# Optimization experiments

Measured on AMD Instinct MI355X. Metric: run time of the kernel, lower is better.

Reference implementation:

```python
import jax, jax.numpy as jnp
import numpy as np

N, L, H, HEADS = 2, 2048, 1024, 16
HD = H // HEADS


def setup_inputs() -> dict:
    key = jax.random.key(0)
    ks = jax.random.split(key, 11)
    s = 1.0 / np.sqrt(H)  # torch Linear-ish init scale
    inp = {
        "H_q": jax.random.normal(ks[0], (N, L, H), jnp.float32),
        "H_k": jax.random.normal(ks[1], (N, L, H), jnp.float32),
        "H_v": jax.random.normal(ks[2], (N, L, H), jnp.float32),
        "W_q": jax.random.normal(ks[3], (H, H), jnp.float32) * s,
        "b_q": jax.random.normal(ks[4], (H,), jnp.float32) * s,
        "W_k": jax.random.normal(ks[5], (H, H), jnp.float32) * s,
        "b_k": jax.random.normal(ks[6], (H,), jnp.float32) * s,
        "W_v": jax.random.normal(ks[7], (H, H), jnp.float32) * s,
        "b_v": jax.random.normal(ks[8], (H,), jnp.float32) * s,
        "W_o": jax.random.normal(ks[9], (H, H), jnp.float32) * s,
        "b_o": jax.random.normal(ks[10], (H,), jnp.float32) * s,
        # causal lookahead mask (L, L): 1 where attending is allowed
        "mask": jnp.tril(jnp.ones((L, L), jnp.int32)),
    }
    return inp


def reference(H_q, H_k, H_v, W_q, b_q, W_k, b_k, W_v, b_v, W_o, b_o, mask):
    n = H_q.shape[0]
    scale = 1.0 / jnp.sqrt(jnp.asarray(H, H_q.dtype))
    # NOTE: faithful to original — raw reshape head split (no transpose),
    # and BOTH Q and K scaled by 1/sqrt(hidden_size).
    Q = ((H_q @ W_q + b_q) * scale).reshape(n, HEADS, L, HD)
    K = ((H_k @ W_k + b_k) * scale).reshape(n, HEADS, L, HD)
    V = (H_v @ W_v + b_v).reshape(n, HEADS, L, HD)
    sims = jnp.einsum("abic,abjc->abij", Q, K)  # (N, heads, L, L)
    neg_inf = jnp.asarray(-jnp.inf, sims.dtype)
    sims = jnp.where(mask[None, None, :, :] == 0, neg_inf, sims)
    # NOTE: softmax over axis=2 (the query axis i), as in the original.
    attn = jax.nn.softmax(sims, axis=2)
    contexts = jnp.einsum("abij,abjc->abic", attn, V)  # (N, heads, L, HD)
    concats = contexts.reshape(n, L, H)
    return concats @ W_o + b_o
```

## Files before the change

### kernel.cpp

```cpp
#include <hip/hip_runtime.h>

#define L 2048
#define HSZ 1024
#define HDIM 64

typedef float f32x4 __attribute__((ext_vector_type(4)));
typedef short short8v __attribute__((ext_vector_type(8)));

static __device__ __forceinline__ unsigned short f2bf(float f) {
    unsigned int u = __builtin_bit_cast(unsigned int, f);
    u += 0x7FFFu + ((u >> 16) & 1u);
    return (unsigned short)(u >> 16);
}
static __device__ __forceinline__ float bf2f(unsigned short u) {
    return __builtin_bit_cast(float, (unsigned int)u << 16);
}
static __device__ __forceinline__ unsigned int cvt_pk_bf16(float lo, float hi) {
    unsigned int r;
    asm("v_cvt_pk_bf16_f32 %0, %1, %2" : "=v"(r) : "v"(lo), "v"(hi));
    return r;
}
static __device__ __forceinline__ void gload_lds16(const void* g, void* l) {
    __builtin_amdgcn_global_load_lds(
        (const __attribute__((address_space(1))) unsigned int*)g,
        (__attribute__((address_space(3))) unsigned int*)l, 16, 0, 0);
}

__global__ __launch_bounds__(256) void wtrans_kernel(
    const float* __restrict__ W0, const float* __restrict__ W1,
    const float* __restrict__ W2, const float* __restrict__ W3,
    unsigned short* __restrict__ Wt4)
{
    const float* W;
    int z = blockIdx.z;
    if (z == 0) W = W0; else if (z == 1) W = W1; else if (z == 2) W = W2; else W = W3;
    unsigned short* T = Wt4 + (size_t)z * HSZ * HSZ;

    __shared__ __align__(16) unsigned short tl[64][72];
    int t = threadIdx.x;
    int k0 = blockIdx.y * 64, n0 = blockIdx.x * 64;

    int kl = t >> 2, nc = (t & 3) * 16;
    const float* src = W + (size_t)(k0 + kl) * HSZ + n0 + nc;
#pragma unroll
    for (int q = 0; q < 4; q++) {
        float4 v = ((const float4*)src)[q];
        tl[kl][nc + q * 4 + 0] = f2bf(v.x);
        tl[kl][nc + q * 4 + 1] = f2bf(v.y);
        tl[kl][nc + q * 4 + 2] = f2bf(v.z);
        tl[kl][nc + q * 4 + 3] = f2bf(v.w);
    }
    __syncthreads();
    int nl = t >> 2, kc = (t & 3) * 16;
    unsigned short tmp[16];
#pragma unroll
    for (int e = 0; e < 16; e++) tmp[e] = tl[kc + e][nl];
    unsigned short* dst = T + (size_t)(n0 + nl) * HSZ + k0 + kc;
    ((uint4*)dst)[0] = *(uint4*)&tmp[0];
    ((uint4*)dst)[1] = *(uint4*)&tmp[8];
}

__global__ __launch_bounds__(256) void hconv_kernel(
    const float* __restrict__ H0, const float* __restrict__ H1,
    const float* __restrict__ H2, unsigned short* __restrict__ Hbf)
{
    int z = blockIdx.y;
    const float* S = (z == 0) ? H0 : (z == 1) ? H1 : H2;
    size_t base = ((size_t)blockIdx.x * 256 + threadIdx.x) * 8;
    unsigned short* D = Hbf + (size_t)z * (4096 * 1024) + base;
    float4 a = *(const float4*)(S + base);
    float4 b = *(const float4*)(S + base + 4);
    unsigned short o[8] = {f2bf(a.x), f2bf(a.y), f2bf(a.z), f2bf(a.w),
                           f2bf(b.x), f2bf(b.y), f2bf(b.z), f2bf(b.w)};
    *(uint4*)D = *(const uint4*)o;
}

__global__ __launch_bounds__(256) void gemm_glds_kernel(
    const unsigned short* __restrict__ A, const unsigned short* __restrict__ B,
    const float* __restrict__ bias0, const float* __restrict__ bias1,
    const float* __restrict__ bias2, float scale01, float scale2,
    unsigned short* __restrict__ outbase)
{
    __shared__ __align__(16) unsigned short As[2][4096];
    __shared__ __align__(16) unsigned short Bs[2][4096];

    int raw = blockIdx.x;
    int xcd = raw & 7, idx = raw >> 3;
    int mb = (xcd * 4 + (idx & 3)) * 128;
    int col = idx >> 2;
    int proj = col >> 3;
    int nb = (col & 7) * 128;

    int t = threadIdx.x;
    int lane = t & 63, w = t >> 6;
    int lr = lane & 15, lg = lane >> 4;
    int wm = (w >> 1) * 64, wn = (w & 1) * 64;

    const unsigned short* Ap = A + (size_t)proj * (4096 * 1024);
    const unsigned short* Bp = B + (size_t)proj * (1024 * 1024);
    const float* bias = (proj == 0) ? bias0 : (proj == 1) ? bias1 : bias2;
    float scale = (proj < 2) ? scale01 : scale2;

    int c0 = w * 64 + lane;
    int r0 = c0 >> 2, e0 = (c0 & 3) * 8;
    int r1 = r0 + 64;
    const unsigned short* gA0 = Ap + (size_t)(mb + r0) * HSZ + e0;
    const unsigned short* gA1 = Ap + (size_t)(mb + r1) * HSZ + e0;
    const unsigned short* gB0 = Bp + (size_t)(nb + r0) * HSZ + e0;
    const unsigned short* gB1 = Bp + (size_t)(nb + r1) * HSZ + e0;

    f32x4 acc[4][4] = {};

    auto stage = [&](int buf, int kt) {
        gload_lds16(gA0 + kt, &As[buf][w * 512]);
        gload_lds16(gA1 + kt, &As[buf][2048 + w * 512]);
        gload_lds16(gB0 + kt, &Bs[buf][w * 512]);
        gload_lds16(gB1 + kt, &Bs[buf][2048 + w * 512]);
    };

    stage(0, 0);
    __syncthreads();

    int buf = 0;
    for (int kt = 0; kt < HSZ; kt += 32) {
        if (kt + 32 < HSZ) stage(buf ^ 1, kt + 32);

        short8v af[4], bfv[4];
#pragma unroll
        for (int s = 0; s < 4; s++) {
            af[s]  = *(const short8v*)&As[buf][(wm + s * 16 + lr) * 32 + lg * 8];
            bfv[s] = *(const short8v*)&Bs[buf][(wn + s * 16 + lr) * 32 + lg * 8];
        }
#pragma unroll
        for (int i = 0; i < 4; i++)
#pragma unroll
            for (int j = 0; j < 4; j++)
                acc[i][j] = __builtin_amdgcn_mfma_f32_16x16x32_bf16(af[i], bfv[j], acc[i][j], 0, 0, 0);
        __syncthreads();
        buf ^= 1;
    }

#pragma unroll
    for (int j = 0; j < 4; j++) {
        int colo = nb + wn + j * 16 + lr;
        float bv = bias[colo];
#pragma unroll
        for (int i = 0; i < 4; i++) {
            int row0 = mb + wm + i * 16 + lg * 4;
#pragma unroll
            for (int rg = 0; rg < 4; rg++) {
                float v = (acc[i][j][rg] + bv) * scale;
                outbase[(size_t)proj * (4096 * 1024) + (size_t)(row0 + rg) * HSZ + colo] = f2bf(v);
            }
        }
    }
}

__global__ __launch_bounds__(256) void gemm_o64_kernel(
    const unsigned short* __restrict__ A, const unsigned short* __restrict__ B,
    const float* __restrict__ bias, float* __restrict__ out)
{
    __shared__ __align__(16) unsigned short As[2][2048];
    __shared__ __align__(16) unsigned short Bs[2][4096];

    int raw = blockIdx.x;
    int xcd = raw & 7, idx = raw >> 3;
    int mb = (xcd * 8 + (idx & 7)) * 64;
    int nb = (idx >> 3) * 128;

    int t = threadIdx.x;
    int lane = t & 63, w = t >> 6;
    int lr = lane & 15, lg = lane >> 4;
    int wm = (w >> 1) * 32, wn = (w & 1) * 64;

    int c0 = w * 64 + lane;
    int r0 = c0 >> 2, e0 = (c0 & 3) * 8;
    const unsigned short* gA0 = A + (size_t)(mb + r0) * HSZ + e0;
    const unsigned short* gB0 = B + (size_t)(nb + r0) * HSZ + e0;
    const unsigned short* gB1 = B + (size_t)(nb + r0 + 64) * HSZ + e0;

    f32x4 acc[2][4] = {};

    auto stage = [&](int buf, int kt) {
        gload_lds16(gA0 + kt, &As[buf][w * 512]);
        gload_lds16(gB0 + kt, &Bs[buf][w * 512]);
        gload_lds16(gB1 + kt, &Bs[buf][2048 + w * 512]);
    };

    stage(0, 0);
    __syncthreads();

    int buf = 0;
    for (int kt = 0; kt < HSZ; kt += 32) {
        if (kt + 32 < HSZ) stage(buf ^ 1, kt + 32);

        short8v af[2], bfv[4];
#pragma unroll
        for (int s = 0; s < 2; s++)
            af[s]  = *(const short8v*)&As[buf][(wm + s * 16 + lr) * 32 + lg * 8];
#pragma unroll
        for (int s = 0; s < 4; s++)
            bfv[s] = *(const short8v*)&Bs[buf][(wn + s * 16 + lr) * 32 + lg * 8];
#pragma unroll
        for (int i = 0; i < 2; i++)
#pragma unroll
            for (int j = 0; j < 4; j++)
                acc[i][j] = __builtin_amdgcn_mfma_f32_16x16x32_bf16(af[i], bfv[j], acc[i][j], 0, 0, 0);
        __syncthreads();
        buf ^= 1;
    }

#pragma unroll
    for (int j = 0; j < 4; j++) {
        int colo = nb + wn + j * 16 + lr;
        float bv = bias[colo];
#pragma unroll
        for (int i = 0; i < 2; i++) {
            int row0 = mb + wm + i * 16 + lg * 4;
#pragma unroll
            for (int rg = 0; rg < 4; rg++)
                out[(size_t)(row0 + rg) * HSZ + colo] = acc[i][j][rg] + bv;
        }
    }
}

template<bool ABF16, bool OUTBF16>
__global__ __launch_bounds__(256) void gemm_bt_kernel(
    const void* __restrict__ Aptr, const unsigned short* __restrict__ Bt,
    const float* __restrict__ bias, float scale, void* __restrict__ outp)
{
    __shared__ __align__(16) unsigned short As[128][40];
    __shared__ __align__(16) unsigned short Bs[128][40];

    int t = threadIdx.x;
    int lane = t & 63, w = t >> 6;
    int lr = lane & 15, lg = lane >> 4;
    int mb = blockIdx.y * 128, nb = blockIdx.x * 128;
    int wm = (w >> 1) * 64, wn = (w & 1) * 64;
    int r = t >> 1, cc = (t & 1) * 16;

    f32x4 acc[4][4] = {};

    for (int kt = 0; kt < HSZ; kt += 32) {
        if (ABF16) {
            const unsigned short* A = (const unsigned short*)Aptr + (size_t)(mb + r) * HSZ + kt + cc;
            *(uint4*)&As[r][cc]     = ((const uint4*)A)[0];
            *(uint4*)&As[r][cc + 8] = ((const uint4*)A)[1];
        } else {
            const float* A = (const float*)Aptr + (size_t)(mb + r) * HSZ + kt + cc;
            unsigned short tmp[16];
#pragma unroll
            for (int q = 0; q < 4; q++) {
                float4 v = ((const float4*)A)[q];
                tmp[q * 4 + 0] = f2bf(v.x); tmp[q * 4 + 1] = f2bf(v.y);
                tmp[q * 4 + 2] = f2bf(v.z); tmp[q * 4 + 3] = f2bf(v.w);
            }
            *(uint4*)&As[r][cc]     = *(uint4*)&tmp[0];
            *(uint4*)&As[r][cc + 8] = *(uint4*)&tmp[8];
        }
        {
            const unsigned short* B = Bt + (size_t)(nb + r) * HSZ + kt + cc;
            *(uint4*)&Bs[r][cc]     = ((const uint4*)B)[0];
            *(uint4*)&Bs[r][cc + 8] = ((const uint4*)B)[1];
        }
        __syncthreads();

        short8v af[4], bf[4];
#pragma unroll
        for (int s = 0; s < 4; s++) af[s] = *(const short8v*)&As[wm + s * 16 + lr][8 * lg];
#pragma unroll
        for (int s = 0; s < 4; s++) bf[s] = *(const short8v*)&Bs[wn + s * 16 + lr][8 * lg];
#pragma unroll
        for (int i = 0; i < 4; i++)
#pragma unroll
            for (int j = 0; j < 4; j++)
                acc[i][j] = __builtin_amdgcn_mfma_f32_16x16x32_bf16(af[i], bf[j], acc[i][j], 0, 0, 0);
        __syncthreads();
    }

#pragma unroll
    for (int j = 0; j < 4; j++) {
        int col = nb + wn + j * 16 + lr;
        float bv = bias[col];
#pragma unroll
        for (int i = 0; i < 4; i++) {
            int row0 = mb + wm + i * 16 + lg * 4;
#pragma unroll
            for (int rg = 0; rg < 4; rg++) {
                float v = (acc[i][j][rg] + bv) * scale;
                if (OUTBF16)
                    ((unsigned short*)outp)[(size_t)(row0 + rg) * HSZ + col] = f2bf(v);
                else
                    ((float*)outp)[(size_t)(row0 + rg) * HSZ + col] = v;
            }
        }
    }
}

__global__ __launch_bounds__(256) void colsum_kernel(
    const unsigned short* __restrict__ Qb, const unsigned short* __restrict__ Kb,
    float* __restrict__ rcpC)
{
    int raw = blockIdx.x;
    int xcd = raw & 7, idx = raw >> 3;
    int head = xcd * 4 + (idx >> 5);
    int jbi = idx & 31;
    if ((idx >> 5) & 1) jbi = 31 - jbi;
    int jb = jbi * 64;
    const unsigned short* Qh = Qb + (size_t)head * L * HDIM;
    const unsigned short* Kh = Kb + (size_t)head * L * HDIM;
    int t = threadIdx.x, lane = t & 63, w = t >> 6;
    int lr = lane & 15, lg = lane >> 4;

    short8v af[4][2];
#pragma unroll
    for (int sj = 0; sj < 4; sj++)
#pragma unroll
        for (int kk = 0; kk < 2; kk++)
            af[sj][kk] = *(const short8v*)&Kh[(size_t)(jb + sj * 16 + lr) * HDIM + kk * 32 + 8 * lg];

    float accs[4][4] = {};

    int it0 = jb + w * 16;
    short8v bc0 = *(const short8v*)&Qh[(size_t)(it0 + lr) * HDIM + 8 * lg];
    short8v bc1 = *(const short8v*)&Qh[(size_t)(it0 + lr) * HDIM + 32 + 8 * lg];

    for (int it = it0; it < L; it += 64) {
        int itn = (it + 64 < L) ? it + 64 : it;
        short8v bn0 = *(const short8v*)&Qh[(size_t)(itn + lr) * HDIM + 8 * lg];
        short8v bn1 = *(const short8v*)&Qh[(size_t)(itn + lr) * HDIM + 32 + 8 * lg];
        if (it == it0) {
            int i = it + lr;
#pragma unroll
            for (int sj = 0; sj < 4; sj++) {
                f32x4 d = {0.0f, 0.0f, 0.0f, 0.0f};
                d = __builtin_amdgcn_mfma_f32_16x16x32_bf16(af[sj][0], bc0, d, 0, 0, 0);
                d = __builtin_amdgcn_mfma_f32_16x16x32_bf16(af[sj][1], bc1, d, 0, 0, 0);
#pragma unroll
                for (int rg = 0; rg < 4; rg++) {
                    int j = jb + sj * 16 + lg * 4 + rg;
                    if (i >= j) accs[sj][rg] += __expf(d[rg]);
                }
            }
        } else {
#pragma unroll
            for (int sj = 0; sj < 4; sj++) {
                f32x4 d = {0.0f, 0.0f, 0.0f, 0.0f};
                d = __builtin_amdgcn_mfma_f32_16x16x32_bf16(af[sj][0], bc0, d, 0, 0, 0);
                d = __builtin_amdgcn_mfma_f32_16x16x32_bf16(af[sj][1], bc1, d, 0, 0, 0);
#pragma unroll
                for (int rg = 0; rg < 4; rg++)
                    accs[sj][rg] += __expf(d[rg]);
            }
        }
        bc0 = bn0; bc1 = bn1;
    }

    __shared__ float part[4][64];
#pragma unroll
    for (int sj = 0; sj < 4; sj++)
#pragma unroll
        for (int rg = 0; rg < 4; rg++) {
            float v = accs[sj][rg];
            v += __shfl_xor(v, 1); v += __shfl_xor(v, 2);
            v += __shfl_xor(v, 4); v += __shfl_xor(v, 8);
            if (lr == 0) part[w][sj * 16 + lg * 4 + rg] = v;
        }
    __syncthreads();
    if (t < 64) {
        float s = part[0][t] + part[1][t] + part[2][t] + part[3][t];
        rcpC[(size_t)head * L + jb + t] = 1.0f / s;
    }
}

__global__ __launch_bounds__(256) void vtrans_kernel(
    const unsigned short* __restrict__ Vb, const float* __restrict__ rcpC,
    unsigned short* __restrict__ Vt)
{
    int p = blockIdx.y;
    int j0 = blockIdx.x * 64;
    const unsigned short* Vp = Vb + (size_t)p * L * HDIM;
    unsigned short* Tp = Vt + (size_t)p * HDIM * L;
    __shared__ __align__(16) unsigned short tl[64][72];
    int t = threadIdx.x;
    int jl = t >> 2, c0 = (t & 3) * 16;
    float rcv = rcpC[(size_t)p * L + j0 + jl];
    const unsigned short* src = Vp + (size_t)(j0 + jl) * HDIM + c0;
    unsigned short raw[16];
    *(uint4*)&raw[0] = ((const uint4*)src)[0];
    *(uint4*)&raw[8] = ((const uint4*)src)[1];
#pragma unroll
    for (int e = 0; e < 16; e++) tl[jl][c0 + e] = f2bf(bf2f(raw[e]) * rcv);
    __syncthreads();
    int cl = t >> 2, jc = (t & 3) * 16;
    unsigned short tmp[16];
#pragma unroll
    for (int e = 0; e < 16; e++) tmp[e] = tl[jc + e][cl];
    unsigned short* dst = Tp + (size_t)cl * L + j0 + jc;
    ((uint4*)dst)[0] = *(uint4*)&tmp[0];
    ((uint4*)dst)[1] = *(uint4*)&tmp[8];
}

__global__ __launch_bounds__(512) void attn_kernel(
    const unsigned short* __restrict__ Qb, const unsigned short* __restrict__ Kb,
    const unsigned short* __restrict__ Vtg, unsigned short* __restrict__ Ctx)
{
    int raw = blockIdx.x;
    int xcd = raw & 7, idx = raw >> 3;
    int head = xcd * 4 + (idx >> 4);
    int jpos = (idx & 15) ^ ((idx >> 5) & 1);
    int qtile = (jpos & 1) ? (jpos >> 1) : (15 - (jpos >> 1));
    int qb = qtile * 128;
    int nt = qb / 64 + 2;

    const unsigned short* Qh = Qb + (size_t)head * L * HDIM;
    const unsigned short* Kh = Kb + (size_t)head * L * HDIM;
    const unsigned short* Vh = Vtg + (size_t)head * HDIM * L;
    unsigned short* Ch = Ctx + (size_t)head * L * HDIM;

    int t = threadIdx.x;
    int lane = t & 63, w = t >> 6;
    int ws = w & 3;
    int w2 = w >> 2;
    int lr = lane & 15, lg = lane >> 4;
    int iw = qb + ws * 32;
    int src0 = ((lane & 16) << 1) + lr;
    int src1 = src0 + 16;
    bool jlow = (lg < 2);

    __shared__ __align__(16) unsigned short SMEM[4][4096];

    int srow = ws * 8 + (lane >> 3);
    int soff = ((lane & 7) ^ (lane >> 3)) * 8;

    auto stageT = [&](int buf, int jt) {
        if (w < 4) {
            gload_lds16(Kh + (size_t)(jt + srow) * HDIM + soff,      &SMEM[buf][ws * 512]);
            gload_lds16(Kh + (size_t)(jt + srow + 32) * HDIM + soff, &SMEM[buf][ws * 512 + 2048]);
        } else {
            gload_lds16(Vh + (size_t)srow * L + jt + soff,           &SMEM[2 + buf][ws * 512]);
            gload_lds16(Vh + (size_t)(srow + 32) * L + jt + soff,    &SMEM[2 + buf][ws * 512 + 2048]);
        }
    };

    short8v bq[2][2];
#pragma unroll
    for (int isub = 0; isub < 2; isub++)
#pragma unroll
        for (int kd = 0; kd < 2; kd++)
            bq[isub][kd] = *(const short8v*)&Qh[(size_t)(iw + isub * 16 + lr) * HDIM + kd * 32 + 8 * lg];

    f32x4 acc[4][2] = {};

    stageT(0, 0);
    __syncthreads();

    for (int tt = 0; tt < nt; ++tt) {
        int buf = tt & 1;
        if (tt + 1 < nt) stageT(buf ^ 1, (tt + 1) * 64);

        int jt32 = tt * 64 + w2 * 32;
        if (jt32 <= iw + 31) {
            short8v ak[2][2];
#pragma unroll
            for (int jsub = 0; jsub < 2; jsub++)
#pragma unroll
                for (int kd = 0; kd < 2; kd++) {
                    int lrow = w2 * 32 + jsub * 16 + lr;
                    int off = lrow * 64 + ((((kd << 2) | lg) ^ (lr & 7)) << 3);
                    ak[jsub][kd] = *(const short8v*)&SMEM[buf][off];
                }
            short8v av[4];
#pragma unroll
            for (int csub = 0; csub < 4; csub++) {
                int vrow = csub * 16 + lr;
                int off = vrow * 64 + ((((w2 << 2) | lg) ^ (lr & 7)) << 3);
                av[csub] = *(const short8v*)&SMEM[2 + buf][off];
            }

            unsigned int pk[2][2][2];
            if (jt32 == iw) {
#pragma unroll
                for (int jsub = 0; jsub < 2; jsub++)
#pragma unroll
                    for (int isub = 0; isub < 2; isub++) {
                        f32x4 s = {0.0f, 0.0f, 0.0f, 0.0f};
                        s = __builtin_amdgcn_mfma_f32_16x16x32_bf16(ak[jsub][0], bq[isub][0], s, 0, 0, 0);
                        s = __builtin_amdgcn_mfma_f32_16x16x32_bf16(ak[jsub][1], bq[isub][1], s, 0, 0, 0);
                        int i = iw + isub * 16 + lr;
                        int jb0 = jt32 + jsub * 16 + lg * 4;
                        float p[4];
#pragma unroll
                        for (int rg = 0; rg < 4; rg++)
                            p[rg] = (jb0 + rg <= i) ? __expf(s[rg]) : 0.0f;
                        pk[jsub][isub][0] = cvt_pk_bf16(p[0], p[1]);
                        pk[jsub][isub][1] = cvt_pk_bf16(p[2], p[3]);
                    }
            } else {
#pragma unroll
                for (int jsub = 0; jsub < 2; jsub++)
#pragma unroll
                    for (int isub = 0; isub < 2; isub++) {
                        f32x4 s = {0.0f, 0.0f, 0.0f, 0.0f};
                        s = __builtin_amdgcn_mfma_f32_16x16x32_bf16(ak[jsub][0], bq[isub][0], s, 0, 0, 0);
                        s = __builtin_amdgcn_mfma_f32_16x16x32_bf16(ak[jsub][1], bq[isub][1], s, 0, 0, 0);
                        pk[jsub][isub][0] = cvt_pk_bf16(__expf(s[0]), __expf(s[1]));
                        pk[jsub][isub][1] = cvt_pk_bf16(__expf(s[2]), __expf(s[3]));
                    }
            }
            __builtin_amdgcn_s_setprio(1);
#pragma unroll
            for (int isub = 0; isub < 2; isub++) {
                int a0 = __shfl((int)pk[0][isub][0], src0);
                int a1 = __shfl((int)pk[0][isub][1], src0);
                int a2 = __shfl((int)pk[0][isub][0], src1);
                int a3 = __shfl((int)pk[0][isub][1], src1);
                int b0 = __shfl((int)pk[1][isub][0], src0);
                int b1 = __shfl((int)pk[1][isub][1], src0);
                int b2 = __shfl((int)pk[1][isub][0], src1);
                int b3 = __shfl((int)pk[1][isub][1], src1);
                int4 wvv;
                wvv.x = jlow ? a0 : b0;
                wvv.y = jlow ? a1 : b1;
                wvv.z = jlow ? a2 : b2;
                wvv.w = jlow ? a3 : b3;
                short8v bp = __builtin_bit_cast(short8v, wvv);
#pragma unroll
                for (int csub = 0; csub < 4; csub++)
                    acc[csub][isub] = __builtin_amdgcn_mfma_f32_16x16x32_bf16(av[csub], bp, acc[csub][isub], 0, 0, 0);
            }
            __builtin_amdgcn_s_setprio(0);
        }
        __syncthreads();
    }

    uint4* red = (uint4*)SMEM;
    if (w >= 4) {
#pragma unroll
        for (int csub = 0; csub < 4; csub++)
#pragma unroll
            for (int isub = 0; isub < 2; isub++)
                red[((ws * 8) + csub * 2 + isub) * 64 + lane] =
                    __builtin_bit_cast(uint4, acc[csub][isub]);
    }
    __syncthreads();
    if (w < 4) {
#pragma unroll
        for (int csub = 0; csub < 4; csub++)
#pragma unroll
            for (int isub = 0; isub < 2; isub++)
                acc[csub][isub] += __builtin_bit_cast(f32x4,
                    red[((ws * 8) + csub * 2 + isub) * 64 + lane]);

#pragma unroll
        for (int csub = 0; csub < 4; csub++)
#pragma unroll
            for (int isub = 0; isub < 2; isub++) {
                int i = iw + isub * 16 + lr;
                int c0 = csub * 16 + lg * 4;
                unsigned short t4[4];
#pragma unroll
                for (int rg = 0; rg < 4; rg++) t4[rg] = f2bf(acc[csub][isub][rg]);
                *(uint2*)&Ch[(size_t)i * HDIM + c0] = *(uint2*)t4;
            }
    }
}

extern "C" void kernel_launch(void* const* d_in, const int* in_sizes, int n_in,
                              void* d_out, int out_size, void* d_ws, size_t ws_size,
                              hipStream_t stream)
{
    const float* H_q = (const float*)d_in[0];
    const float* H_k = (const float*)d_in[1];
    const float* H_v = (const float*)d_in[2];
    const float* W_q = (const float*)d_in[3];
    const float* b_q = (const float*)d_in[4];
    const float* W_k = (const float*)d_in[5];
    const float* b_k = (const float*)d_in[6];
    const float* W_v = (const float*)d_in[7];
    const float* b_v = (const float*)d_in[8];
    const float* W_o = (const float*)d_in[9];
    const float* b_o = (const float*)d_in[10];

    char* ws = (char*)d_ws;
    const size_t MB = (size_t)1 << 20;
    const float scale = 0.03125f;

    if (ws_size >= 60 * MB) {
        unsigned short* Hbf = (unsigned short*)(ws);
        unsigned short* Vt  = (unsigned short*)(ws);
        unsigned short* Ctx = (unsigned short*)(ws + 8 * MB);
        unsigned short* Wt4 = (unsigned short*)(ws + 24 * MB);
        unsigned short* Qb  = (unsigned short*)(ws + 32 * MB);
        unsigned short* Kb  = (unsigned short*)(ws + 40 * MB);
        unsigned short* Vb  = (unsigned short*)(ws + 48 * MB);
        float* rcpC = (float*)(ws + 56 * MB);

        wtrans_kernel<<<dim3(16, 16, 4), 256, 0, stream>>>(W_q, W_k, W_v, W_o, Wt4);
        hconv_kernel<<<dim3(2048, 3), 256, 0, stream>>>(H_q, H_k, H_v, Hbf);
        gemm_glds_kernel<<<768, 256, 0, stream>>>(
            Hbf, Wt4, b_q, b_k, b_v, scale, 1.0f, Qb);
        colsum_kernel<<<1024, 256, 0, stream>>>(Qb, Kb, rcpC);
        vtrans_kernel<<<dim3(32, 32), 256, 0, stream>>>(Vb, rcpC, Vt);
        attn_kernel<<<512, 512, 0, stream>>>(Qb, Kb, Vt, Ctx);
        gemm_o64_kernel<<<512, 256, 0, stream>>>(
            Ctx, Wt4 + (size_t)3 * 1024 * 1024, b_o, (float*)d_out);
    } else {
        unsigned short* Qb  = (unsigned short*)(ws + 0 * MB);
        unsigned short* Kb  = (unsigned short*)(ws + 8 * MB);
        unsigned short* Vt  = (unsigned short*)(ws + 16 * MB);
        unsigned short* Vb  = (unsigned short*)(ws + 24 * MB);
        unsigned short* Ctx = (unsigned short*)(ws + 24 * MB);
        unsigned short* Wt4 = (unsigned short*)(ws + 32 * MB);
        float* rcpC = (float*)(ws + 40 * MB);

        wtrans_kernel<<<dim3(16, 16, 4), 256, 0, stream>>>(W_q, W_k, W_v, W_o, Wt4);
        gemm_bt_kernel<false, true><<<dim3(8, 32), 256, 0, stream>>>(H_q, Wt4, b_q, scale, Qb);
        gemm_bt_kernel<false, true><<<dim3(8, 32), 256, 0, stream>>>(H_k, Wt4 + (size_t)1024 * 1024, b_k, scale, Kb);
        gemm_bt_kernel<false, true><<<dim3(8, 32), 256, 0, stream>>>(H_v, Wt4 + (size_t)2 * 1024 * 1024, b_v, 1.0f, Vb);
        colsum_kernel<<<1024, 256, 0, stream>>>(Qb, Kb, rcpC);
        vtrans_kernel<<<dim3(32, 32), 256, 0, stream>>>(Vb, rcpC, Vt);
        attn_kernel<<<512, 512, 0, stream>>>(Qb, Kb, Vt, Ctx);
        gemm_bt_kernel<true, false><<<dim3(8, 32), 256, 0, stream>>>(Ctx, Wt4 + (size_t)3 * 1024 * 1024, b_o, 1.0f, d_out);
    }
}
```

Measured before the change: 144.7 us.

## Split colsum query range into chunks and combine partial sums atomically

The column-sum kernel now splits each key block's query range into four chunks of 512 rows, one block per chunk. Blocks that fall entirely above the causal diagonal exit early, and partial sums are combined with atomicAdd into a zeroed buffer. The reciprocal moves into vtrans. This is meant to fix load imbalance and low parallelism in colsum, at the cost of an extra memset, atomics and nondeterministic summation order.

```diff
diff --git a/kernel.cpp b/kernel.cpp
--- a/kernel.cpp
+++ b/kernel.cpp
@@ -299,13 +299,14 @@
 
 __global__ __launch_bounds__(256) void colsum_kernel(
     const unsigned short* __restrict__ Qb, const unsigned short* __restrict__ Kb,
-    float* __restrict__ rcpC)
+    float* __restrict__ Csum)
 {
     int raw = blockIdx.x;
     int xcd = raw & 7, idx = raw >> 3;
-    int head = xcd * 4 + (idx >> 5);
-    int jbi = idx & 31;
-    if ((idx >> 5) & 1) jbi = 31 - jbi;
+    int head = xcd * 4 + (idx >> 7);
+    int rem = idx & 127;
+    int jbi = rem >> 2, c = rem & 3;
+    if (c < (jbi >> 3)) return;
     int jb = jbi * 64;
     const unsigned short* Qh = Qb + (size_t)head * L * HDIM;
     const unsigned short* Kh = Kb + (size_t)head * L * HDIM;
@@ -320,40 +321,37 @@
             af[sj][kk] = *(const short8v*)&Kh[(size_t)(jb + sj * 16 + lr) * HDIM + kk * 32 + 8 * lg];
 
     float accs[4][4] = {};
-
-    int it0 = jb + w * 16;
-    short8v bc0 = *(const short8v*)&Qh[(size_t)(it0 + lr) * HDIM + 8 * lg];
-    short8v bc1 = *(const short8v*)&Qh[(size_t)(it0 + lr) * HDIM + 32 + 8 * lg];
-
-    for (int it = it0; it < L; it += 64) {
-        int itn = (it + 64 < L) ? it + 64 : it;
-        short8v bn0 = *(const short8v*)&Qh[(size_t)(itn + lr) * HDIM + 8 * lg];
-        short8v bn1 = *(const short8v*)&Qh[(size_t)(itn + lr) * HDIM + 32 + 8 * lg];
-        if (it == it0) {
-            int i = it + lr;
+    int base = c * 512 + w * 16;
+
+    for (int k = 0; k < 8; ++k) {
+        int it = base + k * 64;
+        if (it + 16 <= jb) continue;
+        short8v bc0 = *(const short8v*)&Qh[(size_t)(it + lr) * HDIM + 8 * lg];
+        short8v bc1 = *(const short8v*)&Qh[(size_t)(it + lr) * HDIM + 32 + 8 * lg];
+        if (it >= jb + 64) {
 #pragma unroll
             for (int sj = 0; sj < 4; sj++) {
                 f32x4 d = {0.0f, 0.0f, 0.0f, 0.0f};
                 d = __builtin_amdgcn_mfma_f32_16x16x32_bf16(af[sj][0], bc0, d, 0, 0, 0);
                 d = __builtin_amdgcn_mfma_f32_16x16x32_bf16(af[sj][1], bc1, d, 0, 0, 0);
 #pragma unroll
+                for (int rg = 0; rg < 4; rg++)
+                    accs[sj][rg] += __expf(d[rg]);
+            }
+        } else {
+            int i = it + lr;
+#pragma unroll
+            for (int sj = 0; sj < 4; sj++) {
+                f32x4 d = {0.0f, 0.0f, 0.0f, 0.0f};
+                d = __builtin_amdgcn_mfma_f32_16x16x32_bf16(af[sj][0], bc0, d, 0, 0, 0);
+                d = __builtin_amdgcn_mfma_f32_16x16x32_bf16(af[sj][1], bc1, d, 0, 0, 0);
+#pragma unroll
                 for (int rg = 0; rg < 4; rg++) {
                     int j = jb + sj * 16 + lg * 4 + rg;
                     if (i >= j) accs[sj][rg] += __expf(d[rg]);
                 }
             }
-        } else {
-#pragma unroll
-            for (int sj = 0; sj < 4; sj++) {
-                f32x4 d = {0.0f, 0.0f, 0.0f, 0.0f};
-                d = __builtin_amdgcn_mfma_f32_16x16x32_bf16(af[sj][0], bc0, d, 0, 0, 0);
-                d = __builtin_amdgcn_mfma_f32_16x16x32_bf16(af[sj][1], bc1, d, 0, 0, 0);
-#pragma unroll
-                for (int rg = 0; rg < 4; rg++)
-                    accs[sj][rg] += __expf(d[rg]);
-            }
-        }
-        bc0 = bn0; bc1 = bn1;
+        }
     }
 
     __shared__ float part[4][64];
@@ -369,12 +367,12 @@
     __syncthreads();
     if (t < 64) {
         float s = part[0][t] + part[1][t] + part[2][t] + part[3][t];
-        rcpC[(size_t)head * L + jb + t] = 1.0f / s;
+        atomicAdd(&Csum[(size_t)head * L + jb + t], s);
     }
 }
 
 __global__ __launch_bounds__(256) void vtrans_kernel(
-    const unsigned short* __restrict__ Vb, const float* __restrict__ rcpC,
+    const unsigned short* __restrict__ Vb, const float* __restrict__ Csum,
     unsigned short* __restrict__ Vt)
 {
     int p = blockIdx.y;
@@ -384,7 +382,7 @@
     __shared__ __align__(16) unsigned short tl[64][72];
     int t = threadIdx.x;
     int jl = t >> 2, c0 = (t & 3) * 16;
-    float rcv = rcpC[(size_t)p * L + j0 + jl];
+    float rcv = 1.0f / Csum[(size_t)p * L + j0 + jl];
     const unsigned short* src = Vp + (size_t)(j0 + jl) * HDIM + c0;
     unsigned short raw[16];
     *(uint4*)&raw[0] = ((const uint4*)src)[0];
@@ -594,14 +592,15 @@
         unsigned short* Qb  = (unsigned short*)(ws + 32 * MB);
         unsigned short* Kb  = (unsigned short*)(ws + 40 * MB);
         unsigned short* Vb  = (unsigned short*)(ws + 48 * MB);
-        float* rcpC = (float*)(ws + 56 * MB);
+        float* Csum = (float*)(ws + 56 * MB);
 
         wtrans_kernel<<<dim3(16, 16, 4), 256, 0, stream>>>(W_q, W_k, W_v, W_o, Wt4);
         hconv_kernel<<<dim3(2048, 3), 256, 0, stream>>>(H_q, H_k, H_v, Hbf);
+        hipMemsetAsync(Csum, 0, (size_t)32 * L * sizeof(float), stream);
         gemm_glds_kernel<<<768, 256, 0, stream>>>(
             Hbf, Wt4, b_q, b_k, b_v, scale, 1.0f, Qb);
-        colsum_kernel<<<1024, 256, 0, stream>>>(Qb, Kb, rcpC);
-        vtrans_kernel<<<dim3(32, 32), 256, 0, stream>>>(Vb, rcpC, Vt);
+        colsum_kernel<<<4096, 256, 0, stream>>>(Qb, Kb, Csum);
+        vtrans_kernel<<<dim3(32, 32), 256, 0, stream>>>(Vb, Csum, Vt);
         attn_kernel<<<512, 512, 0, stream>>>(Qb, Kb, Vt, Ctx);
         gemm_o64_kernel<<<512, 256, 0, stream>>>(
             Ctx, Wt4 + (size_t)3 * 1024 * 1024, b_o, (float*)d_out);
@@ -612,14 +611,15 @@
         unsigned short* Vb  = (unsigned short*)(ws + 24 * MB);
         unsigned short* Ctx = (unsigned short*)(ws + 24 * MB);
         unsigned short* Wt4 = (unsigned short*)(ws + 32 * MB);
-        float* rcpC = (float*)(ws + 40 * MB);
+        float* Csum = (float*)(ws + 40 * MB);
 
         wtrans_kernel<<<dim3(16, 16, 4), 256, 0, stream>>>(W_q, W_k, W_v, W_o, Wt4);
+        hipMemsetAsync(Csum, 0, (size_t)32 * L * sizeof(float), stream);
         gemm_bt_kernel<false, true><<<dim3(8, 32), 256, 0, stream>>>(H_q, Wt4, b_q, scale, Qb);
         gemm_bt_kernel<false, true><<<dim3(8, 32), 256, 0, stream>>>(H_k, Wt4 + (size_t)1024 * 1024, b_k, scale, Kb);
         gemm_bt_kernel<false, true><<<dim3(8, 32), 256, 0, stream>>>(H_v, Wt4 + (size_t)2 * 1024 * 1024, b_v, 1.0f, Vb);
-        colsum_kernel<<<1024, 256, 0, stream>>>(Qb, Kb, rcpC);
-        vtrans_kernel<<<dim3(32, 32), 256, 0, stream>>>(Vb, rcpC, Vt);
+        colsum_kernel<<<4096, 256, 0, stream>>>(Qb, Kb, Csum);
+        vtrans_kernel<<<dim3(32, 32), 256, 0, stream>>>(Vb, Csum, Vt);
         attn_kernel<<<512, 512, 0, stream>>>(Qb, Kb, Vt, Ctx);
         gemm_bt_kernel<true, false><<<dim3(8, 32), 256, 0, stream>>>(Ctx, Wt4 + (size_t)3 * 1024 * 1024, b_o, 1.0f, d_out);
     }
```

Measured after the change: 169.6 us. 1.17x slower.
